# Optimization experiments

Measured on AMD Instinct MI355X. Metric: run time of the kernel, lower is better.

The kernel has to match this reference:

```python
import jax, jax.numpy as jnp
import numpy as np

TOP_K = 2

def setup_inputs() -> dict:
    key = jax.random.key(0)
    k0, k1, k2, k3, k4 = jax.random.split(key, 5)
    B, S, D, H, E = 2, 2048, 1024, 2048, 8
    x = jax.random.normal(k0, (B, S, D), dtype=jnp.float32)
    router_w = jax.random.normal(k1, (D, E), dtype=jnp.float32) * (1.0 / np.sqrt(D))
    wg = jax.random.normal(k2, (E, D, H), dtype=jnp.float32) * (1.0 / np.sqrt(D))
    wu = jax.random.normal(k3, (E, D, H), dtype=jnp.float32) * (1.0 / np.sqrt(D))
    wd = jax.random.normal(k4, (E, H, D), dtype=jnp.float32) * (1.0 / np.sqrt(H))
    return {"x": x, "router_w": router_w, "wg": wg, "wu": wu, "wd": wd}

def reference(x, router_w, wg, wu, wd):
    B, S, D = x.shape
    E = router_w.shape[1]
    xf = x.reshape(-1, D)                                   # [T, D]
    router_logits = xf @ router_w                           # [T, E]
    top_logits, top_idx = jax.lax.top_k(router_logits, TOP_K)
    top_w = jax.nn.softmax(top_logits, axis=-1)             # [T, k]
    # Dense combine weights: W[t, e] = routing weight if e in top-k of t, else 0.
    combine = jnp.sum(jax.nn.one_hot(top_idx, E, dtype=x.dtype) * top_w[..., None], axis=1)  # [T, E]
    # SwiGLU experts, computed for all tokens and masked by the combine weights
    # (mathematically identical to the gather/scatter form in the original).
    gate = jnp.einsum('td,edh->eth', xf, wg)                # [E, T, H]
    up = jnp.einsum('td,edh->eth', xf, wu)                  # [E, T, H]
    fused = jax.nn.silu(gate) * up                          # [E, T, H]
    expert_out = jnp.einsum('eth,ehd->etd', fused, wd)      # [E, T, D]
    y = jnp.einsum('etd,te->td', expert_out, combine)       # [T, D]
    return y.reshape(B, S, D)
```

## Files before the change

### kernel.cpp

```cpp
#include <hip/hip_runtime.h>
#include <hip/hip_bf16.h>

#define T_TOK 4096
#define DDIM  1024
#define HDIM  2048
#define NEXP  8

typedef __attribute__((ext_vector_type(4))) float f32x4;
typedef __attribute__((ext_vector_type(8))) short s16x8;
typedef __hip_bfloat16 bf16;

typedef const void __attribute__((address_space(1))) gvoid;
typedef void __attribute__((address_space(3))) svoid;

__device__ __forceinline__ void gload16(const void* g, void* l) {
    __builtin_amdgcn_global_load_lds((gvoid*)g, (svoid*)l, 16, 0, 0);
}

__device__ __forceinline__ int frag_off(int rr, int kq) {
    int lr = rr >> 1;
    int ch = ((rr & 1) << 2) + (kq >> 3);
    return lr * 64 + (ch ^ (lr & 7)) * 8;
}

__global__ void router_cast_kernel(const float* __restrict__ x, const float* __restrict__ rw,
                                   int* __restrict__ r_e, float* __restrict__ r_w,
                                   bf16* __restrict__ xb) {
    int wave = threadIdx.x >> 6, lane = threadIdx.x & 63;
    int t = blockIdx.x * 4 + wave;
    const float* xr = x + (size_t)t * DDIM;
    bf16* xbr = xb + (size_t)t * DDIM;
    double acc[NEXP];
#pragma unroll
    for (int e = 0; e < NEXP; ++e) acc[e] = 0.0;
#pragma unroll
    for (int c = 0; c < 4; ++c) {
        int d = c * 256 + lane * 4;
        float4 v = *reinterpret_cast<const float4*>(xr + d);
        union { ushort4 u; bf16 h[4]; } o;
        o.h[0] = __float2bfloat16(v.x);
        o.h[1] = __float2bfloat16(v.y);
        o.h[2] = __float2bfloat16(v.z);
        o.h[3] = __float2bfloat16(v.w);
        *reinterpret_cast<ushort4*>(xbr + d) = o.u;
        const float* rw0 = rw + (size_t)d * NEXP;
#pragma unroll
        for (int j = 0; j < 4; ++j) {
            float xv = (&v.x)[j];
            const float* rwr = rw0 + j * NEXP;
#pragma unroll
            for (int e = 0; e < NEXP; ++e) acc[e] += (double)xv * (double)rwr[e];
        }
    }
#pragma unroll
    for (int e = 0; e < NEXP; ++e) {
#pragma unroll
        for (int off = 32; off > 0; off >>= 1) acc[e] += __shfl_down(acc[e], off);
    }
    if (lane == 0) {
        int i0 = 0; double v0 = acc[0];
#pragma unroll
        for (int e = 1; e < NEXP; ++e) if (acc[e] > v0) { v0 = acc[e]; i0 = e; }
        int i1 = -1; double v1 = -1e300;
#pragma unroll
        for (int e = 0; e < NEXP; ++e) { if (e == i0) continue; if (acc[e] > v1) { v1 = acc[e]; i1 = e; } }
        float w0 = 1.0f / (1.0f + expf((float)(v1 - v0)));
        float w1 = 1.0f - w0;
        r_e[2*t]   = i0; r_e[2*t+1] = i1;
        r_w[2*t]   = w0; r_w[2*t+1] = w1;
    }
}

__global__ void binning_kernel(const int* __restrict__ r_e, const float* __restrict__ r_w,
                               int* __restrict__ offs, int* __restrict__ list,
                               float* __restrict__ slot_w) {
    __shared__ int scnt[NEXP], scur[NEXP], soff[NEXP + 1];
    int tid = threadIdx.x;
    if (tid < NEXP) { scnt[tid] = 0; scur[tid] = 0; }
    __syncthreads();
    for (int i = tid; i < 2 * T_TOK; i += 512) atomicAdd(&scnt[r_e[i]], 1);
    __syncthreads();
    if (tid == 0) {
        int s = 0;
        for (int e = 0; e < NEXP; ++e) { soff[e] = s; s += scnt[e]; }
        soff[NEXP] = s;
    }
    __syncthreads();
    if (tid < NEXP + 1) offs[tid] = soff[tid];
    for (int i = tid; i < 2 * T_TOK; i += 512) {
        int e = r_e[i];
        int pos = atomicAdd(&scur[e], 1);
        int slot = soff[e] + pos;
        list[slot] = i >> 1;
        slot_w[slot] = r_w[i];
    }
}

__global__ void transpose_cast_kernel(const float* __restrict__ in, bf16* __restrict__ out,
                                      int R, int C, int rmul, int roff, size_t outE) {
    __shared__ bf16 tile[64][68];
    const float* inp = in + (size_t)blockIdx.z * R * C;
    bf16* outp = out + (size_t)blockIdx.z * outE;
    int r0 = blockIdx.x * 64, c0 = blockIdx.y * 64;
    int tid = threadIdx.x;
#pragma unroll
    for (int i = 0; i < 4; ++i) {
        int idx = i * 256 + tid;
        int r = idx >> 4, c4 = (idx & 15) * 4;
        float4 v = *reinterpret_cast<const float4*>(inp + (size_t)(r0 + r) * C + c0 + c4);
        tile[r][c4 + 0] = __float2bfloat16(v.x);
        tile[r][c4 + 1] = __float2bfloat16(v.y);
        tile[r][c4 + 2] = __float2bfloat16(v.z);
        tile[r][c4 + 3] = __float2bfloat16(v.w);
    }
    __syncthreads();
#pragma unroll
    for (int i = 0; i < 4; ++i) {
        int idx = i * 256 + tid;
        int c = idx >> 4, r4 = (idx & 15) * 4;
        union { ushort4 u; bf16 h[4]; } w;
        w.h[0] = tile[r4 + 0][c];
        w.h[1] = tile[r4 + 1][c];
        w.h[2] = tile[r4 + 2][c];
        w.h[3] = tile[r4 + 3][c];
        *reinterpret_cast<ushort4*>(outp + ((size_t)(c0 + c) * rmul + roff) * R + r0 + r4) = w.u;
    }
}

__global__ __launch_bounds__(256, 2)
void gateup_kernel(const bf16* __restrict__ xb, const bf16* __restrict__ wguT,
                   const int* __restrict__ offs, const int* __restrict__ list,
                   bf16* __restrict__ hbuf) {
    int e = blockIdx.z;
    int base = offs[e];
    int ne = offs[e + 1] - base;
    int m0 = blockIdx.y * 128;
    if (m0 >= ne) return;
    int n0 = blockIdx.x * 128;

    __shared__ bf16 As[2][4096];
    __shared__ bf16 Bs[2][4096];

    int tid = threadIdx.x, lane = tid & 63, wid = tid >> 6;

    const bf16* bbase = wguT + (size_t)e * (2 * HDIM) * DDIM + (size_t)n0 * DDIM;

    const bf16* aS[2]; const bf16* bS[2];
    int sdst[2];
#pragma unroll
    for (int j = 0; j < 2; ++j) {
        int q = wid + j * 4;
        int lr = q * 8 + (lane >> 3);
        int ch = (lane & 7) ^ (lr & 7);
        int rr = 2 * lr + (ch >> 2);
        int koff = (ch & 3) * 8;
        int r = m0 + rr; if (r > ne - 1) r = ne - 1;
        aS[j] = xb + (size_t)list[base + r] * DDIM + koff;
        bS[j] = bbase + (size_t)rr * DDIM + koff;
        sdst[j] = q * 512;
    }

    int rl = lane & 15, kq = 8 * (lane >> 4);
    int wrow = (wid >> 1) * 64;
    int wcol = (wid & 1) * 64;
    int offA[4], offB[4];
#pragma unroll
    for (int mi = 0; mi < 4; ++mi) offA[mi] = frag_off(wrow + mi * 16 + rl, kq);
#pragma unroll
    for (int ni = 0; ni < 4; ++ni) offB[ni] = frag_off(wcol + ni * 16 + rl, kq);

    f32x4 zero4 = {0.f, 0.f, 0.f, 0.f};
    f32x4 acc[4][4];
#pragma unroll
    for (int mi = 0; mi < 4; ++mi)
#pragma unroll
        for (int ni = 0; ni < 4; ++ni) acc[mi][ni] = zero4;

    const int nk = DDIM / 32;

#define GU_STAGE(tt, buf)                                     \
    {                                                         \
        int k0 = (tt) * 32;                                   \
        gload16(aS[0] + k0, &As[buf][sdst[0]]);               \
        gload16(aS[1] + k0, &As[buf][sdst[1]]);               \
        gload16(bS[0] + k0, &Bs[buf][sdst[0]]);               \
        gload16(bS[1] + k0, &Bs[buf][sdst[1]]);               \
    }

    GU_STAGE(0, 0);
    GU_STAGE(1, 1);
    asm volatile("s_waitcnt vmcnt(4)" ::: "memory");
    __builtin_amdgcn_s_barrier();

    for (int t = 0; t < nk; ++t) {
        const bf16* Ab = As[t & 1];
        const bf16* Bb = Bs[t & 1];
        s16x8 a[4], b[4];
#pragma unroll
        for (int mi = 0; mi < 4; ++mi) a[mi] = *reinterpret_cast<const s16x8*>(Ab + offA[mi]);
#pragma unroll
        for (int ni = 0; ni < 4; ++ni) b[ni] = *reinterpret_cast<const s16x8*>(Bb + offB[ni]);
        __builtin_amdgcn_s_setprio(1);
#pragma unroll
        for (int mi = 0; mi < 4; ++mi)
#pragma unroll
            for (int ni = 0; ni < 4; ++ni)
                acc[mi][ni] = __builtin_amdgcn_mfma_f32_16x16x32_bf16(a[mi], b[ni], acc[mi][ni], 0, 0, 0);
        __builtin_amdgcn_s_setprio(0);
        __builtin_amdgcn_sched_barrier(0);
        __builtin_amdgcn_s_barrier();
        if (t + 2 < nk) GU_STAGE(t + 2, t & 1);
        if (t + 1 < nk) {
            if (t + 2 < nk) asm volatile("s_waitcnt vmcnt(4)" ::: "memory");
            else            asm volatile("s_waitcnt vmcnt(0)" ::: "memory");
            __builtin_amdgcn_s_barrier();
        }
    }
#undef GU_STAGE

    int rbase = (lane >> 4) * 4, cbase = lane & 15;
    bool evenlane = (lane & 1) == 0;
#pragma unroll
    for (int mi = 0; mi < 4; ++mi) {
#pragma unroll
        for (int ni = 0; ni < 4; ++ni) {
#pragma unroll
            for (int r = 0; r < 4; ++r) {
                float own = acc[mi][ni][r];
                float oth = __shfl_xor(own, 1);
                int row = m0 + wrow + mi * 16 + rbase + r;
                if (evenlane && row < ne) {
                    float g = own, u = oth;
                    float h = (g / (1.0f + expf(-g))) * u;
                    int hcol = (n0 + wcol + ni * 16 + cbase) >> 1;
                    hbuf[(size_t)(base + row) * HDIM + hcol] = __float2bfloat16(h);
                }
            }
        }
    }
}

__global__ __launch_bounds__(256, 2)
void down_kernel(const bf16* __restrict__ hbuf, const bf16* __restrict__ wdT,
                 const int* __restrict__ offs, const int* __restrict__ list,
                 const float* __restrict__ slot_w, float* __restrict__ y) {
    int e = blockIdx.z;
    int base = offs[e];
    int ne = offs[e + 1] - base;
    int m0 = blockIdx.y * 128;
    if (m0 >= ne) return;
    int n0 = blockIdx.x * 128;

    __shared__ bf16 As[2][4096];
    __shared__ bf16 Bs[2][4096];

    int tid = threadIdx.x, lane = tid & 63, wid = tid >> 6;

    const bf16* bbase = wdT + (size_t)e * DDIM * HDIM + (size_t)n0 * HDIM;

    const bf16* aS[2]; const bf16* bS[2];
    int sdst[2];
#pragma unroll
    for (int j = 0; j < 2; ++j) {
        int q = wid + j * 4;
        int lr = q * 8 + (lane >> 3);
        int ch = (lane & 7) ^ (lr & 7);
        int rr = 2 * lr + (ch >> 2);
        int koff = (ch & 3) * 8;
        int r = m0 + rr; if (r > ne - 1) r = ne - 1;
        aS[j] = hbuf + (size_t)(base + r) * HDIM + koff;
        bS[j] = bbase + (size_t)rr * HDIM + koff;
        sdst[j] = q * 512;
    }

    int rl = lane & 15, kq = 8 * (lane >> 4);
    int wrow = (wid >> 1) * 64;
    int wcol = (wid & 1) * 64;
    int offA[4], offB[4];
#pragma unroll
    for (int mi = 0; mi < 4; ++mi) offA[mi] = frag_off(wrow + mi * 16 + rl, kq);
#pragma unroll
    for (int ni = 0; ni < 4; ++ni) offB[ni] = frag_off(wcol + ni * 16 + rl, kq);

    f32x4 zero4 = {0.f, 0.f, 0.f, 0.f};
    f32x4 acc[4][4];
#pragma unroll
    for (int mi = 0; mi < 4; ++mi)
#pragma unroll
        for (int ni = 0; ni < 4; ++ni) acc[mi][ni] = zero4;

    const int nk = HDIM / 32;

#define DN_STAGE(tt, buf)                                     \
    {                                                         \
        int k0 = (tt) * 32;                                   \
        gload16(aS[0] + k0, &As[buf][sdst[0]]);               \
        gload16(aS[1] + k0, &As[buf][sdst[1]]);               \
        gload16(bS[0] + k0, &Bs[buf][sdst[0]]);               \
        gload16(bS[1] + k0, &Bs[buf][sdst[1]]);               \
    }

    DN_STAGE(0, 0);
    DN_STAGE(1, 1);
    asm volatile("s_waitcnt vmcnt(4)" ::: "memory");
    __builtin_amdgcn_s_barrier();

    for (int t = 0; t < nk; ++t) {
        const bf16* Ab = As[t & 1];
        const bf16* Bb = Bs[t & 1];
        s16x8 a[4], b[4];
#pragma unroll
        for (int mi = 0; mi < 4; ++mi) a[mi] = *reinterpret_cast<const s16x8*>(Ab + offA[mi]);
#pragma unroll
        for (int ni = 0; ni < 4; ++ni) b[ni] = *reinterpret_cast<const s16x8*>(Bb + offB[ni]);
        __builtin_amdgcn_s_setprio(1);
#pragma unroll
        for (int mi = 0; mi < 4; ++mi)
#pragma unroll
            for (int ni = 0; ni < 4; ++ni)
                acc[mi][ni] = __builtin_amdgcn_mfma_f32_16x16x32_bf16(a[mi], b[ni], acc[mi][ni], 0, 0, 0);
        __builtin_amdgcn_s_setprio(0);
        __builtin_amdgcn_sched_barrier(0);
        __builtin_amdgcn_s_barrier();
        if (t + 2 < nk) DN_STAGE(t + 2, t & 1);
        if (t + 1 < nk) {
            if (t + 2 < nk) asm volatile("s_waitcnt vmcnt(4)" ::: "memory");
            else            asm volatile("s_waitcnt vmcnt(0)" ::: "memory");
            __builtin_amdgcn_s_barrier();
        }
    }
#undef DN_STAGE

    int rbase = (lane >> 4) * 4, cbase = lane & 15;
#pragma unroll
    for (int mi = 0; mi < 4; ++mi) {
#pragma unroll
        for (int r = 0; r < 4; ++r) {
            int row = m0 + wrow + mi * 16 + rbase + r;
            if (row < ne) {
                int slot = base + row;
                int tok = list[slot];
                float w = slot_w[slot];
                float* yrow = y + (size_t)tok * DDIM + n0 + wcol + cbase;
#pragma unroll
                for (int ni = 0; ni < 4; ++ni)
                    atomicAdd(yrow + ni * 16, w * acc[mi][ni][r]);
            }
        }
    }
}

extern "C" void kernel_launch(void* const* d_in, const int* in_sizes, int n_in,
                              void* d_out, int out_size, void* d_ws, size_t ws_size,
                              hipStream_t stream) {
    const float* x  = (const float*)d_in[0];
    const float* rw = (const float*)d_in[1];
    const float* wg = (const float*)d_in[2];
    const float* wu = (const float*)d_in[3];
    const float* wd = (const float*)d_in[4];
    float* y = (float*)d_out;

    char* ws = (char*)d_ws;
    int*   r_e    = (int*)  (ws + 0);
    float* r_w    = (float*)(ws + 32768);
    int*   offs   = (int*)  (ws + 65600);
    int*   list   = (int*)  (ws + 65664);
    float* slot_w = (float*)(ws + 98432);
    bf16*  xb     = (bf16*) (ws + 1048576ull);
    bf16*  wguT   = (bf16*) (ws + 16777216ull);
    bf16*  wdT    = (bf16*) (ws + 83886080ull);
    bf16*  hbuf   = (bf16*) (ws + 117440512ull);

    transpose_cast_kernel<<<dim3(DDIM / 64, HDIM / 64, NEXP), 256, 0, stream>>>(
        wg, wguT, DDIM, HDIM, 2, 0, (size_t)2 * HDIM * DDIM);
    transpose_cast_kernel<<<dim3(DDIM / 64, HDIM / 64, NEXP), 256, 0, stream>>>(
        wu, wguT, DDIM, HDIM, 2, 1, (size_t)2 * HDIM * DDIM);
    transpose_cast_kernel<<<dim3(HDIM / 64, DDIM / 64, NEXP), 256, 0, stream>>>(
        wd, wdT, HDIM, DDIM, 1, 0, (size_t)DDIM * HDIM);

    router_cast_kernel<<<dim3(T_TOK / 4), 256, 0, stream>>>(x, rw, r_e, r_w, xb);
    binning_kernel<<<dim3(1), 512, 0, stream>>>(r_e, r_w, offs, list, slot_w);

    hipMemsetAsync(d_out, 0, (size_t)out_size * sizeof(float), stream);

    gateup_kernel<<<dim3(2 * HDIM / 128, T_TOK / 128, NEXP), 256, 0, stream>>>(xb, wguT, offs, list, hbuf);
    down_kernel<<<dim3(DDIM / 128, T_TOK / 128, NEXP), 256, 0, stream>>>(hbuf, wdT, offs, list, slot_w, y);
}
```

Before: 294.9 us.

## Pack expert tiles into a flat padded slot grid and simplify GEMM prefetch

Binning now rounds each expert's segment up to a multiple of 128 rows and also records per-expert counts. The gate/up and down GEMMs launch one flat grid over padded slots, and each block finds its expert with a small search over the offsets. This replaces the old per-expert grid, where most blocks exited immediately because they had no rows. The K-loop pipeline changes from a two-ahead prefetch with partial vmcnt waits to a one-ahead prefetch issued before compute with full waits, which may hide less memory latency. The transpose kernel also writes its tile to LDS as packed 4-element vector stores.

```diff
diff --git a/kernel.cpp b/kernel.cpp
--- a/kernel.cpp
+++ b/kernel.cpp
@@ -5,6 +5,7 @@
 #define DDIM  1024
 #define HDIM  2048
 #define NEXP  8
+#define MAXSLOT 9216
 
 typedef __attribute__((ext_vector_type(4))) float f32x4;
 typedef __attribute__((ext_vector_type(8))) short s16x8;
@@ -72,8 +73,8 @@
 }
 
 __global__ void binning_kernel(const int* __restrict__ r_e, const float* __restrict__ r_w,
-                               int* __restrict__ offs, int* __restrict__ list,
-                               float* __restrict__ slot_w) {
+                               int* __restrict__ offs, int* __restrict__ cnt,
+                               int* __restrict__ list, float* __restrict__ slot_w) {
     __shared__ int scnt[NEXP], scur[NEXP], soff[NEXP + 1];
     int tid = threadIdx.x;
     if (tid < NEXP) { scnt[tid] = 0; scur[tid] = 0; }
@@ -82,11 +83,12 @@
     __syncthreads();
     if (tid == 0) {
         int s = 0;
-        for (int e = 0; e < NEXP; ++e) { soff[e] = s; s += scnt[e]; }
+        for (int e = 0; e < NEXP; ++e) { soff[e] = s; s += (scnt[e] + 127) & ~127; }
         soff[NEXP] = s;
     }
     __syncthreads();
     if (tid < NEXP + 1) offs[tid] = soff[tid];
+    if (tid < NEXP) cnt[tid] = scnt[tid];
     for (int i = tid; i < 2 * T_TOK; i += 512) {
         int e = r_e[i];
         int pos = atomicAdd(&scur[e], 1);
@@ -108,10 +110,12 @@
         int idx = i * 256 + tid;
         int r = idx >> 4, c4 = (idx & 15) * 4;
         float4 v = *reinterpret_cast<const float4*>(inp + (size_t)(r0 + r) * C + c0 + c4);
-        tile[r][c4 + 0] = __float2bfloat16(v.x);
-        tile[r][c4 + 1] = __float2bfloat16(v.y);
-        tile[r][c4 + 2] = __float2bfloat16(v.z);
-        tile[r][c4 + 3] = __float2bfloat16(v.w);
+        union { ushort4 u; bf16 h[4]; } o;
+        o.h[0] = __float2bfloat16(v.x);
+        o.h[1] = __float2bfloat16(v.y);
+        o.h[2] = __float2bfloat16(v.z);
+        o.h[3] = __float2bfloat16(v.w);
+        *reinterpret_cast<ushort4*>(&tile[r][c4]) = o.u;
     }
     __syncthreads();
 #pragma unroll
@@ -127,15 +131,23 @@
     }
 }
 
+__device__ __forceinline__ int find_expert(const int* offs, int slot0) {
+    int e = 0;
+#pragma unroll
+    for (int i = 0; i < NEXP - 1; ++i) e += (offs[e + 1] <= slot0) ? 1 : 0;
+    return e;
+}
+
 __global__ __launch_bounds__(256, 2)
 void gateup_kernel(const bf16* __restrict__ xb, const bf16* __restrict__ wguT,
-                   const int* __restrict__ offs, const int* __restrict__ list,
-                   bf16* __restrict__ hbuf) {
-    int e = blockIdx.z;
+                   const int* __restrict__ offs, const int* __restrict__ cnt,
+                   const int* __restrict__ list, bf16* __restrict__ hbuf) {
+    int slot0 = blockIdx.y * 128;
+    if (slot0 >= offs[NEXP]) return;
+    int e = find_expert(offs, slot0);
     int base = offs[e];
-    int ne = offs[e + 1] - base;
-    int m0 = blockIdx.y * 128;
-    if (m0 >= ne) return;
+    int ne = cnt[e];
+    int m0 = slot0 - base;
     int n0 = blockIdx.x * 128;
 
     __shared__ bf16 As[2][4096];
@@ -188,13 +200,14 @@
     }
 
     GU_STAGE(0, 0);
-    GU_STAGE(1, 1);
-    asm volatile("s_waitcnt vmcnt(4)" ::: "memory");
+    asm volatile("s_waitcnt vmcnt(0)" ::: "memory");
     __builtin_amdgcn_s_barrier();
 
+    int cur = 0;
     for (int t = 0; t < nk; ++t) {
-        const bf16* Ab = As[t & 1];
-        const bf16* Bb = Bs[t & 1];
+        if (t + 1 < nk) GU_STAGE(t + 1, cur ^ 1);
+        const bf16* Ab = As[cur];
+        const bf16* Bb = Bs[cur];
         s16x8 a[4], b[4];
 #pragma unroll
         for (int mi = 0; mi < 4; ++mi) a[mi] = *reinterpret_cast<const s16x8*>(Ab + offA[mi]);
@@ -208,13 +221,11 @@
                 acc[mi][ni] = __builtin_amdgcn_mfma_f32_16x16x32_bf16(a[mi], b[ni], acc[mi][ni], 0, 0, 0);
         __builtin_amdgcn_s_setprio(0);
         __builtin_amdgcn_sched_barrier(0);
-        __builtin_amdgcn_s_barrier();
-        if (t + 2 < nk) GU_STAGE(t + 2, t & 1);
         if (t + 1 < nk) {
-            if (t + 2 < nk) asm volatile("s_waitcnt vmcnt(4)" ::: "memory");
-            else            asm volatile("s_waitcnt vmcnt(0)" ::: "memory");
+            asm volatile("s_waitcnt vmcnt(0)" ::: "memory");
             __builtin_amdgcn_s_barrier();
         }
+        cur ^= 1;
     }
 #undef GU_STAGE
 
@@ -242,13 +253,15 @@
 
 __global__ __launch_bounds__(256, 2)
 void down_kernel(const bf16* __restrict__ hbuf, const bf16* __restrict__ wdT,
-                 const int* __restrict__ offs, const int* __restrict__ list,
-                 const float* __restrict__ slot_w, float* __restrict__ y) {
-    int e = blockIdx.z;
+                 const int* __restrict__ offs, const int* __restrict__ cnt,
+                 const int* __restrict__ list, const float* __restrict__ slot_w,
+                 float* __restrict__ y) {
+    int slot0 = blockIdx.y * 128;
+    if (slot0 >= offs[NEXP]) return;
+    int e = find_expert(offs, slot0);
     int base = offs[e];
-    int ne = offs[e + 1] - base;
-    int m0 = blockIdx.y * 128;
-    if (m0 >= ne) return;
+    int ne = cnt[e];
+    int m0 = slot0 - base;
     int n0 = blockIdx.x * 128;
 
     __shared__ bf16 As[2][4096];
@@ -301,13 +314,14 @@
     }
 
     DN_STAGE(0, 0);
-    DN_STAGE(1, 1);
-    asm volatile("s_waitcnt vmcnt(4)" ::: "memory");
+    asm volatile("s_waitcnt vmcnt(0)" ::: "memory");
     __builtin_amdgcn_s_barrier();
 
+    int cur = 0;
     for (int t = 0; t < nk; ++t) {
-        const bf16* Ab = As[t & 1];
-        const bf16* Bb = Bs[t & 1];
+        if (t + 1 < nk) DN_STAGE(t + 1, cur ^ 1);
+        const bf16* Ab = As[cur];
+        const bf16* Bb = Bs[cur];
         s16x8 a[4], b[4];
 #pragma unroll
         for (int mi = 0; mi < 4; ++mi) a[mi] = *reinterpret_cast<const s16x8*>(Ab + offA[mi]);
@@ -321,13 +335,11 @@
                 acc[mi][ni] = __builtin_amdgcn_mfma_f32_16x16x32_bf16(a[mi], b[ni], acc[mi][ni], 0, 0, 0);
         __builtin_amdgcn_s_setprio(0);
         __builtin_amdgcn_sched_barrier(0);
-        __builtin_amdgcn_s_barrier();
-        if (t + 2 < nk) DN_STAGE(t + 2, t & 1);
         if (t + 1 < nk) {
-            if (t + 2 < nk) asm volatile("s_waitcnt vmcnt(4)" ::: "memory");
-            else            asm volatile("s_waitcnt vmcnt(0)" ::: "memory");
+            asm volatile("s_waitcnt vmcnt(0)" ::: "memory");
             __builtin_amdgcn_s_barrier();
         }
+        cur ^= 1;
     }
 #undef DN_STAGE
 
@@ -364,8 +376,9 @@
     int*   r_e    = (int*)  (ws + 0);
     float* r_w    = (float*)(ws + 32768);
     int*   offs   = (int*)  (ws + 65600);
-    int*   list   = (int*)  (ws + 65664);
-    float* slot_w = (float*)(ws + 98432);
+    int*   cnt    = (int*)  (ws + 65544 + 96);
+    int*   list   = (int*)  (ws + 65664 + 128);
+    float* slot_w = (float*)(ws + 65664 + 128 + 4 * MAXSLOT);
     bf16*  xb     = (bf16*) (ws + 1048576ull);
     bf16*  wguT   = (bf16*) (ws + 16777216ull);
     bf16*  wdT    = (bf16*) (ws + 83886080ull);
@@ -379,10 +392,12 @@
         wd, wdT, HDIM, DDIM, 1, 0, (size_t)DDIM * HDIM);
 
     router_cast_kernel<<<dim3(T_TOK / 4), 256, 0, stream>>>(x, rw, r_e, r_w, xb);
-    binning_kernel<<<dim3(1), 512, 0, stream>>>(r_e, r_w, offs, list, slot_w);
+    binning_kernel<<<dim3(1), 512, 0, stream>>>(r_e, r_w, offs, cnt, list, slot_w);
 
     hipMemsetAsync(d_out, 0, (size_t)out_size * sizeof(float), stream);
 
-    gateup_kernel<<<dim3(2 * HDIM / 128, T_TOK / 128, NEXP), 256, 0, stream>>>(xb, wguT, offs, list, hbuf);
-    down_kernel<<<dim3(DDIM / 128, T_TOK / 128, NEXP), 256, 0, stream>>>(hbuf, wdT, offs, list, slot_w, y);
-}
+    gateup_kernel<<<dim3(2 * HDIM / 128, MAXSLOT / 128, 1), 256, 0, stream>>>(
+        xb, wguT, offs, cnt, list, hbuf);
+    down_kernel<<<dim3(DDIM / 128, MAXSLOT / 128, 1), 256, 0, stream>>>(
+        hbuf, wdT, offs, cnt, list, slot_w, y);
+}
```

After: 289.0 us. 2.0% less time.
